# Kernel optimization log

Hardware: AMD Instinct MI355X
Metric: run time of the kernel (lower is better)

## Reference

```python
import jax, jax.numpy as jnp
import numpy as np

DIM = 768
HEADS = 12
B, N = 4, 2048

def setup_inputs() -> dict:
    key = jax.random.key(0)
    ks = jax.random.split(key, 6)
    x = jax.random.normal(ks[0], (B, N, DIM), dtype=jnp.float32)
    ln_w = jnp.ones((DIM,), dtype=jnp.float32)
    ln_b = jnp.zeros((DIM,), dtype=jnp.float32)
    # nn.Linear(dim, 3*dim, bias=False): weight shape [3*dim, dim]
    w_qkv = jax.random.normal(ks[1], (3 * DIM, DIM), dtype=jnp.float32) * (DIM ** -0.5)
    w_out = jax.random.normal(ks[2], (DIM, DIM), dtype=jnp.float32) * (DIM ** -0.5)
    b_out = jnp.zeros((DIM,), dtype=jnp.float32)
    return {"x": x, "ln_w": ln_w, "ln_b": ln_b, "w_qkv": w_qkv, "w_out": w_out, "b_out": b_out}

def reference(x, ln_w, ln_b, w_qkv, w_out, b_out):
    h = HEADS
    d = x.shape[-1] // h
    scale = d ** -0.5
    # LayerNorm (eps=1e-5, torch default)
    mu = jnp.mean(x, axis=-1, keepdims=True)
    var = jnp.mean(jnp.square(x - mu), axis=-1, keepdims=True)
    xn = (x - mu) * jax.lax.rsqrt(var + 1e-5) * ln_w + ln_b
    # QKV projection (no bias), then split heads: b n (h d) -> b h n d
    qkv = jnp.einsum('bnc,fc->bnf', xn, w_qkv)  # [B,N,3*DIM]
    q, k, v = jnp.split(qkv, 3, axis=-1)
    def split_heads(t):
        b, n, _ = t.shape
        return t.reshape(b, n, h, d).transpose(0, 2, 1, 3)  # b h n d
    q, k, v = map(split_heads, (q, k, v))
    scores = jnp.einsum('bhid,bhjd->bhij', q, k) * scale  # [B,H,N,N]
    attn = jax.nn.softmax(scores, axis=-1)
    out = jnp.einsum('bhij,bhjd->bhid', attn, v)  # [B,H,N,d]
    out = out.transpose(0, 2, 1, 3).reshape(x.shape)  # b n (h d)
    return jnp.einsum('bnc,oc->bno', out, w_out) + b_out
```

## Files before the change

kernel.cpp:

```cpp
#include <hip/hip_runtime.h>
#include <hip/hip_bf16.h>
#include <stdint.h>


#define DIMC   768
#define HEADS  12
#define BBATCH 4
#define SEQ    2048
#define HD     64
#define NBH    (BBATCH*HEADS)
#define ROWS   (BBATCH*SEQ)
#define NQKV   (3*DIMC)

typedef __attribute__((ext_vector_type(8)))  short        short8;
typedef __attribute__((ext_vector_type(4)))  float        f32x4;
typedef __attribute__((ext_vector_type(16))) float        f32x16;
typedef __attribute__((ext_vector_type(4)))  unsigned int uint4v;

__device__ __forceinline__ unsigned short f2bf(float f) {
  union { float f; unsigned int u; } v; v.f = f;
  unsigned int r = v.u + 0x7fffu + ((v.u >> 16) & 1u);
  return (unsigned short)(r >> 16);
}

__device__ __forceinline__ void gload16(const void* g, void* l) {
  __builtin_amdgcn_global_load_lds(
      (const __attribute__((address_space(1))) void*)g,
      (__attribute__((address_space(3))) void*)l, 16, 0, 0);
}

__device__ __forceinline__ float fast_exp2(float x) {
  float r;
  asm("v_exp_f32 %0, %1" : "=v"(r) : "v"(x));
  return r;
}

__global__ void conv_kernel(const float* __restrict__ s, unsigned short* __restrict__ d, int n4) {
  int i = blockIdx.x * 256 + threadIdx.x;
  if (i >= n4) return;
  float4 v = ((const float4*)s)[i];
  unsigned long long pk =
      (unsigned long long)f2bf(v.x) |
      ((unsigned long long)f2bf(v.y) << 16) |
      ((unsigned long long)f2bf(v.z) << 32) |
      ((unsigned long long)f2bf(v.w) << 48);
  ((unsigned long long*)d)[i] = pk;
}

__global__ void ln_kernel(const float* __restrict__ x, const float* __restrict__ w,
                          const float* __restrict__ b, unsigned short* __restrict__ xn) {
  const int row = blockIdx.x;
  const int t = threadIdx.x;
  const float* xr = x + (size_t)row * DIMC;
  float v0 = xr[t], v1 = xr[t + 256], v2 = xr[t + 512];
  float s = v0 + v1 + v2;
  float q = v0 * v0 + v1 * v1 + v2 * v2;
  #pragma unroll
  for (int o = 32; o; o >>= 1) { s += __shfl_down(s, o, 64); q += __shfl_down(q, o, 64); }
  __shared__ float ls[4], lq[4];
  const int wid = t >> 6, lane = t & 63;
  if (lane == 0) { ls[wid] = s; lq[wid] = q; }
  __syncthreads();
  s = ls[0] + ls[1] + ls[2] + ls[3];
  q = lq[0] + lq[1] + lq[2] + lq[3];
  const float mu = s * (1.0f / DIMC);
  const float var = q * (1.0f / DIMC) - mu * mu;
  const float rs = rsqrtf(var + 1e-5f);
  unsigned short* o = xn + (size_t)row * DIMC;
  o[t]       = f2bf((v0 - mu) * rs * w[t]       + b[t]);
  o[t + 256] = f2bf((v1 - mu) * rs * w[t + 256] + b[t + 256]);
  o[t + 512] = f2bf((v2 - mu) * rs * w[t + 512] + b[t + 512]);
}

template<int EPI>
__global__ __launch_bounds__(256, 2) void gemm_bt(
    const unsigned short* __restrict__ A,
    const unsigned short* __restrict__ Bw,
    void* __restrict__ outp,
    const float* __restrict__ bias,
    unsigned short* __restrict__ vout,
    int M, int N, int K) {
  __shared__ unsigned short lA[128 * 32];
  __shared__ unsigned short lB[128 * 32];
  const int nt_cnt = N >> 7;
  const int nwg = (int)gridDim.x;
  const int bid = (int)blockIdx.x;
  const int idx = (bid & 7) * (nwg >> 3) + (bid >> 3);
  const int mt = idx / nt_cnt, nt = idx % nt_cnt;
  const int t = (int)threadIdx.x;
  const int w = t >> 6, lane = t & 63;
  const int wr = w >> 1, wc = w & 1;
  const int fr = lane & 15, kg = lane >> 4;
  const int m0 = mt << 7, n0 = nt << 7;

  const int c1 = (w << 6) + lane;
  const int c2 = c1 + 256;
  const unsigned short* gA1 = A  + (size_t)(m0 + (c1 >> 2)) * K + ((c1 & 3) << 3);
  const unsigned short* gA2 = A  + (size_t)(m0 + (c2 >> 2)) * K + ((c2 & 3) << 3);
  const unsigned short* gB1 = Bw + (size_t)(n0 + (c1 >> 2)) * K + ((c1 & 3) << 3);
  const unsigned short* gB2 = Bw + (size_t)(n0 + (c2 >> 2)) * K + ((c2 & 3) << 3);
  char* lA1 = (char*)lA + (w << 10);
  char* lA2 = (char*)lA + 4096 + (w << 10);
  char* lB1 = (char*)lB + (w << 10);
  char* lB2 = (char*)lB + 4096 + (w << 10);

  f32x4 acc[4][4];
  #pragma unroll
  for (int mi = 0; mi < 4; ++mi)
    #pragma unroll
    for (int ni = 0; ni < 4; ++ni)
      #pragma unroll
      for (int r = 0; r < 4; ++r) acc[mi][ni][r] = 0.f;

  for (int kt = 0; kt < K; kt += 32) {
    gload16(gA1 + kt, lA1);
    gload16(gA2 + kt, lA2);
    gload16(gB1 + kt, lB1);
    gload16(gB2 + kt, lB2);
    __syncthreads();
    short8 af[4], bfr[4];
    #pragma unroll
    for (int mi = 0; mi < 4; ++mi)
      af[mi] = *(const short8*)(lA + ((wr << 6) + (mi << 4) + fr) * 32 + (kg << 3));
    #pragma unroll
    for (int ni = 0; ni < 4; ++ni)
      bfr[ni] = *(const short8*)(lB + ((wc << 6) + (ni << 4) + fr) * 32 + (kg << 3));
    #pragma unroll
    for (int mi = 0; mi < 4; ++mi)
      #pragma unroll
      for (int ni = 0; ni < 4; ++ni)
        acc[mi][ni] = __builtin_amdgcn_mfma_f32_16x16x32_bf16(af[mi], bfr[ni], acc[mi][ni], 0, 0, 0);
    __syncthreads();
  }

  if (EPI == 2 && n0 >= 2 * DIMC) {
    #pragma unroll
    for (int mi = 0; mi < 4; ++mi) {
      const int row0 = m0 + (wr << 6) + (mi << 4) + (kg << 2);
      const int bb = row0 >> 11;
      const int nb = row0 & 2047;
      #pragma unroll
      for (int ni = 0; ni < 4; ++ni) {
        const int c = n0 - 2 * DIMC + (wc << 6) + (ni << 4) + fr;
        const int vrow = ((bb * HEADS + (c >> 6)) << 6) + (c & 63);
        unsigned long long pk =
            (unsigned long long)f2bf(acc[mi][ni][0]) |
            ((unsigned long long)f2bf(acc[mi][ni][1]) << 16) |
            ((unsigned long long)f2bf(acc[mi][ni][2]) << 32) |
            ((unsigned long long)f2bf(acc[mi][ni][3]) << 48);
        *(unsigned long long*)(vout + (size_t)vrow * SEQ + nb) = pk;
      }
    }
  } else {
    #pragma unroll
    for (int mi = 0; mi < 4; ++mi) {
      const int row0 = m0 + (wr << 6) + (mi << 4) + (kg << 2);
      #pragma unroll
      for (int ni = 0; ni < 4; ++ni) {
        const int col = n0 + (wc << 6) + (ni << 4) + fr;
        #pragma unroll
        for (int r = 0; r < 4; ++r) {
          if (EPI == 1)
            ((float*)outp)[(size_t)(row0 + r) * N + col] = acc[mi][ni][r] + bias[col];
          else
            ((unsigned short*)outp)[(size_t)(row0 + r) * N + col] = f2bf(acc[mi][ni][r]);
        }
      }
    }
  }
}

__global__ __launch_bounds__(256, 2) void attn_kernel(
    const unsigned short* __restrict__ qkv,
    const unsigned short* __restrict__ vt,
    unsigned short* __restrict__ outp) {
  __shared__ unsigned char lds[32768];
  const int bid = (int)blockIdx.x;
  const int bh = bid % NBH;
  const int qt = bid / NBH;
  const int b = bh / HEADS, h = bh % HEADS;
  const int t = (int)threadIdx.x;
  const int w = t >> 6, l = t & 63;
  const int i = l & 31, hi = l >> 5;
  const float CSC = 0.18033688011112042f;

  const unsigned short* qp = qkv + (size_t)(b * SEQ + (qt << 7) + (w << 5) + i) * NQKV + h * HD + (hi << 3);
  short8 qf[4];
  #pragma unroll
  for (int g = 0; g < 4; ++g) qf[g] = *(const short8*)(qp + (g << 4));

  const int c1 = (w << 6) + l, c2 = c1 + 256;
  const int r1 = c1 >> 3, r2 = c2 >> 3;
  const int sc1 = ((c1 & 7) ^ (r1 & 7)) << 3;
  const int sc2 = ((c2 & 7) ^ (r2 & 7)) << 3;
  const unsigned short* gK1 = qkv + (size_t)(b * SEQ + r1) * NQKV + DIMC + h * HD + sc1;
  const unsigned short* gK2 = qkv + (size_t)(b * SEQ + r2) * NQKV + DIMC + h * HD + sc2;
  const unsigned short* gV1 = vt + (size_t)((bh << 6) + r1) * SEQ + sc1;
  const unsigned short* gV2 = vt + (size_t)((bh << 6) + r2) * SEQ + sc2;
  unsigned char* dK = lds + (w << 10);
  unsigned char* dV = lds + 16384 + (w << 10);

  const uint4v onesu = {0x3F803F80u, 0x3F803F80u, 0x3F803F80u, 0x3F803F80u};
  const short8 onesb = __builtin_bit_cast(short8, onesu);

  f32x16 acc0, acc1, accS;
  #pragma unroll
  for (int r = 0; r < 16; ++r) { acc0[r] = 0.f; acc1[r] = 0.f; accS[r] = 0.f; }
  float m_run = -1e30f;

#define STAGE(BUF, KV0) do {                                       \
    gload16(gK1 + (size_t)(KV0) * NQKV, dK + (BUF) * 8192);        \
    gload16(gK2 + (size_t)(KV0) * NQKV, dK + (BUF) * 8192 + 4096); \
    gload16(gV1 + (KV0), dV + (BUF) * 8192);                       \
    gload16(gV2 + (KV0), dV + (BUF) * 8192 + 4096);                \
  } while (0)

#define PACK(SV, PBA, PBB) do {                                                     \
    float p_[16];                                                                   \
    _Pragma("unroll")                                                               \
    for (int r = 0; r < 16; ++r) p_[r] = fast_exp2(__builtin_fmaf(SV[r], CSC, -nmc));\
    unsigned int W_[8];                                                             \
    _Pragma("unroll")                                                               \
    for (int wd = 0; wd < 8; ++wd) {                                                \
      unsigned int pk;                                                              \
      asm("v_cvt_pk_bf16_f32 %0, %1, %2" : "=v"(pk)                                 \
          : "v"(p_[2 * wd]), "v"(p_[2 * wd + 1]));                                  \
      W_[wd] = pk;                                                                  \
    }                                                                               \
    unsigned int r02_ = (unsigned int)__shfl_xor((int)(hi ? W_[0] : W_[2]), 32, 64);\
    unsigned int r13_ = (unsigned int)__shfl_xor((int)(hi ? W_[1] : W_[3]), 32, 64);\
    unsigned int r46_ = (unsigned int)__shfl_xor((int)(hi ? W_[4] : W_[6]), 32, 64);\
    unsigned int r57_ = (unsigned int)__shfl_xor((int)(hi ? W_[5] : W_[7]), 32, 64);\
    uint4v u0_, u1_;                                                                \
    u0_.x = hi ? r02_ : W_[0]; u0_.y = hi ? r13_ : W_[1];                           \
    u0_.z = hi ? W_[2] : r02_; u0_.w = hi ? W_[3] : r13_;                           \
    u1_.x = hi ? r46_ : W_[4]; u1_.y = hi ? r57_ : W_[5];                           \
    u1_.z = hi ? W_[6] : r46_; u1_.w = hi ? W_[7] : r57_;                           \
    PBA = __builtin_bit_cast(short8, u0_);                                          \
    PBB = __builtin_bit_cast(short8, u1_);                                          \
  } while (0)

  STAGE(0, 0);
  __syncthreads();

  const int swz = (i & 7) << 4;
  for (int kt = 0; kt < 32; ++kt) {
    const int cur = kt & 1;
    if (kt < 31) STAGE(cur ^ 1, (kt + 1) << 6);
    const unsigned char* Kc = lds + cur * 8192;
    const unsigned char* Vc = lds + 16384 + cur * 8192;

    f32x16 s0, s1;
    #pragma unroll
    for (int r = 0; r < 16; ++r) { s0[r] = 0.f; s1[r] = 0.f; }
    #pragma unroll
    for (int g = 0; g < 4; ++g) {
      const int ch = ((g << 1) | hi) << 4;
      short8 k0 = *(const short8*)(Kc + (i << 7) + (ch ^ swz));
      short8 k1 = *(const short8*)(Kc + ((32 + i) << 7) + (ch ^ swz));
      s0 = __builtin_amdgcn_mfma_f32_32x32x16_bf16(k0, qf[g], s0, 0, 0, 0);
      s1 = __builtin_amdgcn_mfma_f32_32x32x16_bf16(k1, qf[g], s1, 0, 0, 0);
    }
    float mtA = fmaxf(fmaxf(s0[0], s0[1]), s0[2]);
    #pragma unroll
    for (int r = 3; r < 15; r += 2) mtA = fmaxf(fmaxf(mtA, s0[r]), s0[r + 1]);
    mtA = fmaxf(mtA, s0[15]);
    float mtB = fmaxf(fmaxf(s1[0], s1[1]), s1[2]);
    #pragma unroll
    for (int r = 3; r < 15; r += 2) mtB = fmaxf(fmaxf(mtB, s1[r]), s1[r + 1]);
    mtB = fmaxf(mtB, s1[15]);
    float mt = fmaxf(mtA, mtB);
    mt = fmaxf(mt, __shfl_xor(mt, 32, 64));
    if (!__all(mt <= m_run + 44.3614f)) {
      const float mn = fmaxf(m_run, mt);
      const float frs = fast_exp2((m_run - mn) * CSC);
      m_run = mn;
      acc0 = acc0 * frs;
      acc1 = acc1 * frs;
      accS = accS * frs;
    }
    const float nmc = m_run * CSC;
    short8 pb0, pb1, pb2, pb3;
    PACK(s0, pb0, pb1);
    PACK(s1, pb2, pb3);
    {
      const int ch0 = (hi) << 4, ch1 = (2 | hi) << 4, ch2 = (4 | hi) << 4, ch3 = (6 | hi) << 4;
      short8 v00 = *(const short8*)(Vc + (i << 7) + (ch0 ^ swz));
      short8 v10 = *(const short8*)(Vc + ((32 + i) << 7) + (ch0 ^ swz));
      acc0 = __builtin_amdgcn_mfma_f32_32x32x16_bf16(v00, pb0, acc0, 0, 0, 0);
      acc1 = __builtin_amdgcn_mfma_f32_32x32x16_bf16(v10, pb0, acc1, 0, 0, 0);
      accS = __builtin_amdgcn_mfma_f32_32x32x16_bf16(onesb, pb0, accS, 0, 0, 0);
      short8 v01 = *(const short8*)(Vc + (i << 7) + (ch1 ^ swz));
      short8 v11 = *(const short8*)(Vc + ((32 + i) << 7) + (ch1 ^ swz));
      acc0 = __builtin_amdgcn_mfma_f32_32x32x16_bf16(v01, pb1, acc0, 0, 0, 0);
      acc1 = __builtin_amdgcn_mfma_f32_32x32x16_bf16(v11, pb1, acc1, 0, 0, 0);
      accS = __builtin_amdgcn_mfma_f32_32x32x16_bf16(onesb, pb1, accS, 0, 0, 0);
      short8 v02 = *(const short8*)(Vc + (i << 7) + (ch2 ^ swz));
      short8 v12 = *(const short8*)(Vc + ((32 + i) << 7) + (ch2 ^ swz));
      acc0 = __builtin_amdgcn_mfma_f32_32x32x16_bf16(v02, pb2, acc0, 0, 0, 0);
      acc1 = __builtin_amdgcn_mfma_f32_32x32x16_bf16(v12, pb2, acc1, 0, 0, 0);
      accS = __builtin_amdgcn_mfma_f32_32x32x16_bf16(onesb, pb2, accS, 0, 0, 0);
      short8 v03 = *(const short8*)(Vc + (i << 7) + (ch3 ^ swz));
      short8 v13 = *(const short8*)(Vc + ((32 + i) << 7) + (ch3 ^ swz));
      acc0 = __builtin_amdgcn_mfma_f32_32x32x16_bf16(v03, pb3, acc0, 0, 0, 0);
      acc1 = __builtin_amdgcn_mfma_f32_32x32x16_bf16(v13, pb3, acc1, 0, 0, 0);
      accS = __builtin_amdgcn_mfma_f32_32x32x16_bf16(onesb, pb3, accS, 0, 0, 0);
    }
    __syncthreads();
  }
#undef STAGE
#undef PACK

  const float inv = 1.0f / accS[0];
  unsigned char* T = lds + (w << 12);
  #pragma unroll
  for (int r = 0; r < 16; ++r) {
    const int drow = (r & 3) + ((r >> 2) << 3) + (hi << 2);
    *(unsigned short*)(T + i * 128 + ((drow * 2) ^ ((i & 7) << 4))) = f2bf(acc0[r] * inv);
    const int d1 = drow + 32;
    *(unsigned short*)(T + i * 128 + ((d1 * 2) ^ ((i & 7) << 4))) = f2bf(acc1[r] * inv);
  }
  __syncthreads();
  const int q = l >> 1, half = l & 1;
  unsigned short* orow = outp + (size_t)(b * SEQ + (qt << 7) + (w << 5) + q) * DIMC + h * HD + half * 32;
  #pragma unroll
  for (int cc = 0; cc < 4; ++cc) {
    int byte = q * 128 + ((((half << 6) + (cc << 4))) ^ ((q & 7) << 4));
    short8 v = *(const short8*)(T + byte);
    *(short8*)(orow + (cc << 3)) = v;
  }
}

extern "C" void kernel_launch(void* const* d_in, const int* in_sizes, int n_in,
                              void* d_out, int out_size, void* d_ws, size_t ws_size,
                              hipStream_t stream) {
  const float* x    = (const float*)d_in[0];
  const float* lnw  = (const float*)d_in[1];
  const float* lnb  = (const float*)d_in[2];
  const float* wqkv = (const float*)d_in[3];
  const float* wout = (const float*)d_in[4];
  const float* bout = (const float*)d_in[5];
  float* out = (float*)d_out;

  char* ws = (char*)d_ws;
  unsigned short* xn   = (unsigned short*)(ws);
  unsigned short* wqb  = (unsigned short*)(ws + 12582912);
  unsigned short* wob  = (unsigned short*)(ws + 16121856);
  unsigned short* qkvb = (unsigned short*)(ws + 17301504);
  unsigned short* vtb  = (unsigned short*)(ws + 55050240);
  unsigned short* ao   = (unsigned short*)(ws + 67633152);

  conv_kernel<<<(NQKV * DIMC / 4 + 255) / 256, 256, 0, stream>>>(wqkv, wqb, NQKV * DIMC / 4);
  conv_kernel<<<(DIMC * DIMC / 4 + 255) / 256, 256, 0, stream>>>(wout, wob, DIMC * DIMC / 4);
  ln_kernel<<<ROWS, 256, 0, stream>>>(x, lnw, lnb, xn);
  gemm_bt<2><<<(ROWS / 128) * (NQKV / 128), 256, 0, stream>>>(xn, wqb, (void*)qkvb, nullptr, vtb, ROWS, NQKV, DIMC);
  attn_kernel<<<NBH * (SEQ / 128), 256, 0, stream>>>(qkvb, vtb, ao);
  gemm_bt<1><<<(ROWS / 128) * (DIMC / 128), 256, 0, stream>>>(ao, wob, (void*)out, bout, nullptr, ROWS, DIMC, DIMC);
}
```

Measured before the change: 161.3 us.

## Fuse weight conversion into LayerNorm launch and halve attention block size

```diff
diff --git a/kernel.cpp b/kernel.cpp
--- a/kernel.cpp
+++ b/kernel.cpp
@@ -35,9 +35,8 @@
   return r;
 }
 
-__global__ void conv_kernel(const float* __restrict__ s, unsigned short* __restrict__ d, int n4) {
-  int i = blockIdx.x * 256 + threadIdx.x;
-  if (i >= n4) return;
+__device__ __forceinline__ void conv_body(const float* __restrict__ s,
+                                          unsigned short* __restrict__ d, int i) {
   float4 v = ((const float4*)s)[i];
   unsigned long long pk =
       (unsigned long long)f2bf(v.x) |
@@ -47,17 +46,25 @@
   ((unsigned long long*)d)[i] = pk;
 }
 
-__global__ void ln_kernel(const float* __restrict__ x, const float* __restrict__ w,
-                          const float* __restrict__ b, unsigned short* __restrict__ xn) {
-  const int row = blockIdx.x;
-  const int t = threadIdx.x;
+__global__ void prep_kernel(const float* __restrict__ x, const float* __restrict__ w,
+                            const float* __restrict__ b, unsigned short* __restrict__ xn,
+                            const float* __restrict__ wqkv, unsigned short* __restrict__ wqb,
+                            const float* __restrict__ wout, unsigned short* __restrict__ wob) {
+  __shared__ float ls[4], lq[4];
+  const int bid = (int)blockIdx.x;
+  const int t = (int)threadIdx.x;
+  if (bid >= ROWS) {
+    if (bid < ROWS + 1728) conv_body(wqkv, wqb, (bid - ROWS) * 256 + t);
+    else                   conv_body(wout, wob, (bid - ROWS - 1728) * 256 + t);
+    return;
+  }
+  const int row = bid;
   const float* xr = x + (size_t)row * DIMC;
   float v0 = xr[t], v1 = xr[t + 256], v2 = xr[t + 512];
   float s = v0 + v1 + v2;
   float q = v0 * v0 + v1 * v1 + v2 * v2;
   #pragma unroll
   for (int o = 32; o; o >>= 1) { s += __shfl_down(s, o, 64); q += __shfl_down(q, o, 64); }
-  __shared__ float ls[4], lq[4];
   const int wid = t >> 6, lane = t & 63;
   if (lane == 0) { ls[wid] = s; lq[wid] = q; }
   __syncthreads();
@@ -170,7 +177,7 @@
   }
 }
 
-__global__ __launch_bounds__(256, 2) void attn_kernel(
+__global__ __launch_bounds__(128, 2) void attn_kernel(
     const unsigned short* __restrict__ qkv,
     const unsigned short* __restrict__ vt,
     unsigned short* __restrict__ outp) {
@@ -184,19 +191,25 @@
   const int i = l & 31, hi = l >> 5;
   const float CSC = 0.18033688011112042f;
 
-  const unsigned short* qp = qkv + (size_t)(b * SEQ + (qt << 7) + (w << 5) + i) * NQKV + h * HD + (hi << 3);
+  const unsigned short* qp = qkv + (size_t)(b * SEQ + (qt << 6) + (w << 5) + i) * NQKV + h * HD + (hi << 3);
   short8 qf[4];
   #pragma unroll
   for (int g = 0; g < 4; ++g) qf[g] = *(const short8*)(qp + (g << 4));
 
-  const int c1 = (w << 6) + l, c2 = c1 + 256;
-  const int r1 = c1 >> 3, r2 = c2 >> 3;
-  const int sc1 = ((c1 & 7) ^ (r1 & 7)) << 3;
-  const int sc2 = ((c2 & 7) ^ (r2 & 7)) << 3;
-  const unsigned short* gK1 = qkv + (size_t)(b * SEQ + r1) * NQKV + DIMC + h * HD + sc1;
-  const unsigned short* gK2 = qkv + (size_t)(b * SEQ + r2) * NQKV + DIMC + h * HD + sc2;
-  const unsigned short* gV1 = vt + (size_t)((bh << 6) + r1) * SEQ + sc1;
-  const unsigned short* gV2 = vt + (size_t)((bh << 6) + r2) * SEQ + sc2;
+  const int c0 = t, c1 = t + 128, c2 = t + 256, c3 = t + 384;
+  const int r0 = c0 >> 3, r1 = c1 >> 3, r2 = c2 >> 3, r3 = c3 >> 3;
+  const int s0c = ((c0 & 7) ^ (r0 & 7)) << 3;
+  const int s1c = ((c1 & 7) ^ (r1 & 7)) << 3;
+  const int s2c = ((c2 & 7) ^ (r2 & 7)) << 3;
+  const int s3c = ((c3 & 7) ^ (r3 & 7)) << 3;
+  const unsigned short* gK0 = qkv + (size_t)(b * SEQ + r0) * NQKV + DIMC + h * HD + s0c;
+  const unsigned short* gK1 = qkv + (size_t)(b * SEQ + r1) * NQKV + DIMC + h * HD + s1c;
+  const unsigned short* gK2 = qkv + (size_t)(b * SEQ + r2) * NQKV + DIMC + h * HD + s2c;
+  const unsigned short* gK3 = qkv + (size_t)(b * SEQ + r3) * NQKV + DIMC + h * HD + s3c;
+  const unsigned short* gV0 = vt + (size_t)((bh << 6) + r0) * SEQ + s0c;
+  const unsigned short* gV1 = vt + (size_t)((bh << 6) + r1) * SEQ + s1c;
+  const unsigned short* gV2 = vt + (size_t)((bh << 6) + r2) * SEQ + s2c;
+  const unsigned short* gV3 = vt + (size_t)((bh << 6) + r3) * SEQ + s3c;
   unsigned char* dK = lds + (w << 10);
   unsigned char* dV = lds + 16384 + (w << 10);
 
@@ -208,11 +221,15 @@
   for (int r = 0; r < 16; ++r) { acc0[r] = 0.f; acc1[r] = 0.f; accS[r] = 0.f; }
   float m_run = -1e30f;
 
-#define STAGE(BUF, KV0) do {                                       \
-    gload16(gK1 + (size_t)(KV0) * NQKV, dK + (BUF) * 8192);        \
-    gload16(gK2 + (size_t)(KV0) * NQKV, dK + (BUF) * 8192 + 4096); \
-    gload16(gV1 + (KV0), dV + (BUF) * 8192);                       \
-    gload16(gV2 + (KV0), dV + (BUF) * 8192 + 4096);                \
+#define STAGE(BUF, KV0) do {                                          \
+    gload16(gK0 + (size_t)(KV0) * NQKV, dK + (BUF) * 8192);           \
+    gload16(gK1 + (size_t)(KV0) * NQKV, dK + (BUF) * 8192 + 2048);    \
+    gload16(gK2 + (size_t)(KV0) * NQKV, dK + (BUF) * 8192 + 4096);    \
+    gload16(gK3 + (size_t)(KV0) * NQKV, dK + (BUF) * 8192 + 6144);    \
+    gload16(gV0 + (KV0), dV + (BUF) * 8192);                          \
+    gload16(gV1 + (KV0), dV + (BUF) * 8192 + 2048);                   \
+    gload16(gV2 + (KV0), dV + (BUF) * 8192 + 4096);                   \
+    gload16(gV3 + (KV0), dV + (BUF) * 8192 + 6144);                   \
   } while (0)
 
 #define PACK(SV, PBA, PBB) do {                                                     \
@@ -322,7 +339,7 @@
   }
   __syncthreads();
   const int q = l >> 1, half = l & 1;
-  unsigned short* orow = outp + (size_t)(b * SEQ + (qt << 7) + (w << 5) + q) * DIMC + h * HD + half * 32;
+  unsigned short* orow = outp + (size_t)(b * SEQ + (qt << 6) + (w << 5) + q) * DIMC + h * HD + half * 32;
   #pragma unroll
   for (int cc = 0; cc < 4; ++cc) {
     int byte = q * 128 + ((((half << 6) + (cc << 4))) ^ ((q & 7) << 4));
@@ -350,10 +367,8 @@
   unsigned short* vtb  = (unsigned short*)(ws + 55050240);
   unsigned short* ao   = (unsigned short*)(ws + 67633152);
 
-  conv_kernel<<<(NQKV * DIMC / 4 + 255) / 256, 256, 0, stream>>>(wqkv, wqb, NQKV * DIMC / 4);
-  conv_kernel<<<(DIMC * DIMC / 4 + 255) / 256, 256, 0, stream>>>(wout, wob, DIMC * DIMC / 4);
-  ln_kernel<<<ROWS, 256, 0, stream>>>(x, lnw, lnb, xn);
+  prep_kernel<<<ROWS + 1728 + 576, 256, 0, stream>>>(x, lnw, lnb, xn, wqkv, wqb, wout, wob);
   gemm_bt<2><<<(ROWS / 128) * (NQKV / 128), 256, 0, stream>>>(xn, wqb, (void*)qkvb, nullptr, vtb, ROWS, NQKV, DIMC);
-  attn_kernel<<<NBH * (SEQ / 128), 256, 0, stream>>>(qkvb, vtb, ao);
+  attn_kernel<<<NBH * (SEQ / 64), 128, 0, stream>>>(qkvb, vtb, ao);
   gemm_bt<1><<<(ROWS / 128) * (DIMC / 128), 256, 0, stream>>>(ao, wob, (void*)out, bout, nullptr, ROWS, DIMC, DIMC);
 }
```

After: 188.1 us. 1.17x slower.
